# Optimization experiments

Hardware: AMD Instinct MI355X
Metric: run time of the kernel (lower is better)

## Reference

```python
import jax, jax.numpy as jnp
import numpy as np

N_NODES = 50000
N_HEDGES = 100000
E = 800000          # node->node incidences and hedge->node incidences
F_IN = 128
F_H = 64
F_OUT = 128


def setup_inputs() -> dict:
    key = jax.random.key(0)
    ks = jax.random.split(key, 10)
    node_features = jax.random.normal(ks[0], (N_NODES, F_IN), jnp.float32)
    hedge_features = jax.random.normal(ks[1], (N_HEDGES, F_H), jnp.float32)
    node_senders = jax.random.randint(ks[2], (E,), 0, N_NODES)
    node_receivers = jnp.sort(jax.random.randint(ks[3], (E,), 0, N_NODES))
    node_convolution = jax.random.uniform(ks[4], (E, 1), jnp.float32)
    hedge2node_senders = jax.random.randint(ks[5], (E,), 0, N_HEDGES)
    hedge2node_receivers = jnp.sort(jax.random.randint(ks[6], (E,), 0, N_NODES))
    hedge2node_convolution = jax.random.uniform(ks[7], (E, 1), jnp.float32)
    # eqx.nn.Linear-style uniform init: U(-1/sqrt(fan_in), 1/sqrt(fan_in))
    lim1 = 1.0 / np.sqrt(F_IN)
    lim2 = 1.0 / np.sqrt(F_H)
    W_msg = jax.random.uniform(ks[8], (F_OUT, F_IN), jnp.float32, -lim1, lim1)
    b_msg = jnp.zeros((F_OUT,), jnp.float32)
    W_scale = jax.random.uniform(ks[9], (F_OUT, F_H), jnp.float32, -lim2, lim2)
    b_scale = jnp.zeros((F_OUT,), jnp.float32)
    return dict(node_features=node_features, hedge_features=hedge_features,
                node_senders=node_senders, node_receivers=node_receivers,
                node_convolution=node_convolution,
                hedge2node_senders=hedge2node_senders,
                hedge2node_receivers=hedge2node_receivers,
                hedge2node_convolution=hedge2node_convolution,
                W_msg=W_msg, b_msg=b_msg, W_scale=W_scale, b_scale=b_scale)


def reference(node_features, hedge_features, node_senders, node_receivers,
              node_convolution, hedge2node_senders, hedge2node_receivers,
              hedge2node_convolution, W_msg, b_msg, W_scale, b_scale):
    # pipeline 1: gather node senders -> linear -> scale -> scatter-add to receivers
    sender_features = node_features[node_senders]                 # [E, F_IN]
    messages = sender_features @ W_msg.T + b_msg                  # [E, F_OUT]
    gathered_messages = jax.ops.segment_sum(
        node_convolution * messages, node_receivers, num_segments=N_NODES)
    # pipeline 2: gather hedge senders -> linear -> scale -> scatter-add to receivers
    hedge_sender_features = hedge_features[hedge2node_senders]    # [E, F_H]
    hedge_messages = hedge_sender_features @ W_scale.T + b_scale  # [E, F_OUT]
    gathered_scaling = jax.ops.segment_sum(
        hedge2node_convolution * hedge_messages, hedge2node_receivers,
        num_segments=N_NODES)
    return jnp.tanh(gathered_scaling * gathered_messages)         # [N_NODES, F_OUT]
```

## Files before the change

### kernel.cpp

```cpp
#include <hip/hip_runtime.h>

#define N_NODES   50000
#define N_HEDGES  100000
#define E_EDGES   800000
#define F_IN      128
#define F_H       64
#define F_OUT     128

typedef __attribute__((ext_vector_type(8))) short short8;
typedef __attribute__((ext_vector_type(4))) float f32x4;
typedef _Float16 half2_t __attribute__((ext_vector_type(2)));
typedef _Float16 half4_t __attribute__((ext_vector_type(4)));

__device__ __forceinline__ unsigned short f2bf(float f) {
    unsigned int u = __float_as_uint(f);
    return (unsigned short)((u + 0x7fffu + ((u >> 16) & 1u)) >> 16);
}
__device__ __forceinline__ float bf2f(unsigned short h) {
    return __uint_as_float(((unsigned int)h) << 16);
}

#define OFF_ITEMS (2 * (N_NODES + 1) + F_OUT * (F_IN + F_H))
#define OFF_B     ((OFF_ITEMS + 255) / 256)
#define CONV_NODE_F4  (N_NODES * 32)
#define CONV_HEDGE_F4 (N_HEDGES * 16)
#define CONV_B    ((CONV_NODE_F4 + CONV_HEDGE_F4 + 255) / 256)

__global__ __launch_bounds__(256)
void offsets_kernel(const int* __restrict__ recv1, const int* __restrict__ recv2,
                    int* __restrict__ offs1, int* __restrict__ offs2,
                    const float* __restrict__ Wm, const float* __restrict__ Wsc,
                    unsigned short* __restrict__ wmhi, unsigned short* __restrict__ wmlo,
                    unsigned short* __restrict__ wshi, unsigned short* __restrict__ wslo,
                    const float* __restrict__ nf, const float* __restrict__ hf,
                    _Float16* __restrict__ nfH, _Float16* __restrict__ hfH) {
    if (blockIdx.x < OFF_B) {
        int t = blockIdx.x * blockDim.x + threadIdx.x;
        const int total = N_NODES + 1;
        if (t < total) {
            int r = t, lo = 0, hi = E_EDGES;
            while (lo < hi) { int mid = (lo + hi) >> 1; if (recv1[mid] < r) lo = mid + 1; else hi = mid; }
            offs1[r] = lo;
        } else if (t < 2 * total) {
            int r = t - total, lo = 0, hi = E_EDGES;
            while (lo < hi) { int mid = (lo + hi) >> 1; if (recv2[mid] < r) lo = mid + 1; else hi = mid; }
            offs2[r] = lo;
        } else if (t < OFF_ITEMS) {
            int idx = t - 2 * total;
            if (idx < F_OUT * F_IN) {
                float f = Wm[idx];
                unsigned short h = f2bf(f);
                wmhi[idx] = h; wmlo[idx] = f2bf(f - bf2f(h));
            } else {
                int i2 = idx - F_OUT * F_IN;
                float f = Wsc[i2];
                unsigned short h = f2bf(f);
                wshi[i2] = h; wslo[i2] = f2bf(f - bf2f(h));
            }
        }
    } else {
        int idx = (blockIdx.x - OFF_B) * 256 + threadIdx.x;
        if (idx < CONV_NODE_F4) {
            float4 v = *(const float4*)(nf + (size_t)idx * 4);
            half4_t h = { (_Float16)v.x, (_Float16)v.y, (_Float16)v.z, (_Float16)v.w };
            *(half4_t*)(nfH + (size_t)idx * 4) = h;
        } else {
            int i2 = idx - CONV_NODE_F4;
            if (i2 < CONV_HEDGE_F4) {
                float4 v = *(const float4*)(hf + (size_t)i2 * 4);
                half4_t h = { (_Float16)v.x, (_Float16)v.y, (_Float16)v.z, (_Float16)v.w };
                *(half4_t*)(hfH + (size_t)i2 * 4) = h;
            }
        }
    }
}

__device__ __forceinline__ void node4(const _Float16* base, const int* __restrict__ snd,
                                      const float* __restrict__ cv, int i,
                                      float& a0, float& a1, float& cs) {
    int   s0 = snd[i],  s1 = snd[i+1], s2 = snd[i+2], s3 = snd[i+3];
    float c0 = cv[i],   c1 = cv[i+1],  c2 = cv[i+2],  c3 = cv[i+3];
    half2_t v0 = *(const half2_t*)(base + (size_t)s0 * F_IN);
    half2_t v1 = *(const half2_t*)(base + (size_t)s1 * F_IN);
    half2_t v2 = *(const half2_t*)(base + (size_t)s2 * F_IN);
    half2_t v3 = *(const half2_t*)(base + (size_t)s3 * F_IN);
    a0 += c0 * (float)v0.x; a1 += c0 * (float)v0.y;
    a0 += c1 * (float)v1.x; a1 += c1 * (float)v1.y;
    a0 += c2 * (float)v2.x; a1 += c2 * (float)v2.y;
    a0 += c3 * (float)v3.x; a1 += c3 * (float)v3.y;
    cs += c0 + c1 + c2 + c3;
}
__device__ __forceinline__ void node1(const _Float16* base, const int* __restrict__ snd,
                                      const float* __restrict__ cv, int i,
                                      float& a0, float& a1, float& cs) {
    int sn = snd[i]; float c = cv[i];
    half2_t v = *(const half2_t*)(base + (size_t)sn * F_IN);
    a0 += c * (float)v.x; a1 += c * (float)v.y; cs += c;
}
__device__ __forceinline__ void hedge4(const _Float16* base, const int* __restrict__ snd,
                                       const float* __restrict__ cv, int i,
                                       float& a, float& cs) {
    int   s0 = snd[i],  s1 = snd[i+1], s2 = snd[i+2], s3 = snd[i+3];
    float c0 = cv[i],   c1 = cv[i+1],  c2 = cv[i+2],  c3 = cv[i+3];
    float v0 = (float)base[(size_t)s0 * F_H], v1 = (float)base[(size_t)s1 * F_H];
    float v2 = (float)base[(size_t)s2 * F_H], v3 = (float)base[(size_t)s3 * F_H];
    a += c0 * v0; a += c1 * v1; a += c2 * v2; a += c3 * v3;
    cs += c0 + c1 + c2 + c3;
}
__device__ __forceinline__ void hedge1(const _Float16* base, const int* __restrict__ snd,
                                       const float* __restrict__ cv, int i,
                                       float& a, float& cs) {
    int sn = snd[i]; float c = cv[i];
    a += c * (float)base[(size_t)sn * F_H]; cs += c;
}
__device__ __forceinline__ void pack_node(char* a1pack, int node, int lane, float a0, float a1) {
    unsigned short h0 = f2bf(a0), h1 = f2bf(a1);
    unsigned short l0 = f2bf(a0 - bf2f(h0)), l1 = f2bf(a1 - bf2f(h1));
    *(unsigned int*)(a1pack + (size_t)node * 512 + lane * 4)       = (unsigned)h0 | ((unsigned)h1 << 16);
    *(unsigned int*)(a1pack + (size_t)node * 512 + 256 + lane * 4) = (unsigned)l0 | ((unsigned)l1 << 16);
}
__device__ __forceinline__ void pack_hedge(char* a2pack, int node, int lane, float a) {
    unsigned short h = f2bf(a);
    unsigned short l = f2bf(a - bf2f(h));
    ((unsigned short*)(a2pack + (size_t)node * 256))[lane]       = h;
    ((unsigned short*)(a2pack + (size_t)node * 256 + 128))[lane] = l;
}

__global__ __launch_bounds__(256)
void gather_fused(const _Float16* __restrict__ nfH, const _Float16* __restrict__ hfH,
                  const int* __restrict__ snd1, const float* __restrict__ cv1,
                  const int* __restrict__ o1,
                  const int* __restrict__ snd2, const float* __restrict__ cv2,
                  const int* __restrict__ o2,
                  char* a1pack, char* __restrict__ a2pack,
                  float* __restrict__ cs1o, float* __restrict__ cs2o) {
    const int lane = threadIdx.x & 63;
    const int wid  = threadIdx.x >> 6;
    const int NB   = N_NODES / 8;

    if (blockIdx.x < NB) {
        const int nodeA = blockIdx.x * 8 + wid * 2;
        const int nodeB = nodeA + 1;
        const _Float16* base = nfH + lane * 2;
        int iA = o1[nodeA];
        int eA = o1[nodeB];
        int iB = eA;
        int eB = o1[nodeB + 1];
        float aA0 = 0.f, aA1 = 0.f, csA = 0.f;
        float aB0 = 0.f, aB1 = 0.f, csB = 0.f;
        while (iA + 4 <= eA && iB + 4 <= eB) {
            node4(base, snd1, cv1, iA, aA0, aA1, csA);
            node4(base, snd1, cv1, iB, aB0, aB1, csB);
            iA += 4; iB += 4;
        }
        for (; iA + 4 <= eA; iA += 4) node4(base, snd1, cv1, iA, aA0, aA1, csA);
        for (; iA < eA; ++iA)         node1(base, snd1, cv1, iA, aA0, aA1, csA);
        for (; iB + 4 <= eB; iB += 4) node4(base, snd1, cv1, iB, aB0, aB1, csB);
        for (; iB < eB; ++iB)         node1(base, snd1, cv1, iB, aB0, aB1, csB);
        pack_node(a1pack, nodeA, lane, aA0, aA1);
        pack_node(a1pack, nodeB, lane, aB0, aB1);
        if (lane == 0) { cs1o[nodeA] = csA; cs1o[nodeB] = csB; }
    } else {
        const int nodeA = (blockIdx.x - NB) * 8 + wid * 2;
        const int nodeB = nodeA + 1;
        const _Float16* base = hfH + lane;
        int iA = o2[nodeA];
        int eA = o2[nodeB];
        int iB = eA;
        int eB = o2[nodeB + 1];
        float aA = 0.f, csA = 0.f, aB = 0.f, csB = 0.f;
        while (iA + 4 <= eA && iB + 4 <= eB) {
            hedge4(base, snd2, cv2, iA, aA, csA);
            hedge4(base, snd2, cv2, iB, aB, csB);
            iA += 4; iB += 4;
        }
        for (; iA + 4 <= eA; iA += 4) hedge4(base, snd2, cv2, iA, aA, csA);
        for (; iA < eA; ++iA)         hedge1(base, snd2, cv2, iA, aA, csA);
        for (; iB + 4 <= eB; iB += 4) hedge4(base, snd2, cv2, iB, aB, csB);
        for (; iB < eB; ++iB)         hedge1(base, snd2, cv2, iB, aB, csB);
        pack_hedge(a2pack, nodeA, lane, aA);
        pack_hedge(a2pack, nodeB, lane, aB);
        if (lane == 0) { cs2o[nodeA] = csA; cs2o[nodeB] = csB; }
    }
}

__global__ __launch_bounds__(256)
void gather_nodes_kernel(const float* __restrict__ nf, const int* __restrict__ senders,
                         const float* __restrict__ conv, const int* __restrict__ offs,
                         char* a1pack, float* __restrict__ csum_out) {
    const int lane = threadIdx.x & 63;
    const int node = blockIdx.x * 4 + (threadIdx.x >> 6);
    const int s = offs[node], e = offs[node + 1];
    float a0 = 0.f, a1 = 0.f, cs = 0.f;
    const float* base = nf + lane * 2;
    int i = s;
    for (; i + 4 <= e; i += 4) {
        int   s0 = senders[i],   s1 = senders[i+1], s2 = senders[i+2], s3 = senders[i+3];
        float c0 = conv[i],      c1 = conv[i+1],    c2 = conv[i+2],    c3 = conv[i+3];
        float2 v0 = *(const float2*)(base + s0 * F_IN);
        float2 v1 = *(const float2*)(base + s1 * F_IN);
        float2 v2 = *(const float2*)(base + s2 * F_IN);
        float2 v3 = *(const float2*)(base + s3 * F_IN);
        a0 += c0 * v0.x; a1 += c0 * v0.y;
        a0 += c1 * v1.x; a1 += c1 * v1.y;
        a0 += c2 * v2.x; a1 += c2 * v2.y;
        a0 += c3 * v3.x; a1 += c3 * v3.y;
        cs += c0 + c1 + c2 + c3;
    }
    for (; i < e; ++i) {
        int sn = senders[i]; float c = conv[i];
        float2 v = *(const float2*)(base + sn * F_IN);
        a0 += c * v.x; a1 += c * v.y; cs += c;
    }
    unsigned short h0 = f2bf(a0), h1 = f2bf(a1);
    unsigned short l0 = f2bf(a0 - bf2f(h0)), l1 = f2bf(a1 - bf2f(h1));
    unsigned int* hp = (unsigned int*)(a1pack + (size_t)node * 512);
    unsigned int* lp = (unsigned int*)(a1pack + (size_t)node * 512 + 256);
    hp[lane] = (unsigned int)h0 | ((unsigned int)h1 << 16);
    lp[lane] = (unsigned int)l0 | ((unsigned int)l1 << 16);
    if (lane == 0) csum_out[node] = cs;
}

__global__ __launch_bounds__(256)
void gather_hedges_kernel(const float* __restrict__ hf, const int* __restrict__ senders,
                          const float* __restrict__ conv, const int* __restrict__ offs,
                          char* __restrict__ a2pack, float* __restrict__ csum_out) {
    const int lane = threadIdx.x & 63;
    const int node = blockIdx.x * 4 + (threadIdx.x >> 6);
    const int s = offs[node], e = offs[node + 1];
    float a = 0.f, cs = 0.f;
    const float* base = hf + lane;
    int i = s;
    for (; i + 4 <= e; i += 4) {
        int   s0 = senders[i],   s1 = senders[i+1], s2 = senders[i+2], s3 = senders[i+3];
        float c0 = conv[i],      c1 = conv[i+1],    c2 = conv[i+2],    c3 = conv[i+3];
        float v0 = base[s0 * F_H], v1 = base[s1 * F_H];
        float v2 = base[s2 * F_H], v3 = base[s3 * F_H];
        a += c0 * v0; a += c1 * v1; a += c2 * v2; a += c3 * v3;
        cs += c0 + c1 + c2 + c3;
    }
    for (; i < e; ++i) {
        int sn = senders[i]; float c = conv[i];
        a += c * base[sn * F_H]; cs += c;
    }
    unsigned short h = f2bf(a);
    unsigned short l = f2bf(a - bf2f(h));
    ((unsigned short*)(a2pack + (size_t)node * 256))[lane]       = h;
    ((unsigned short*)(a2pack + (size_t)node * 256 + 128))[lane] = l;
    if (lane == 0) csum_out[node] = cs;
}

__global__ __launch_bounds__(256)
void gemm_tanh_kernel(const char* a1pack,
                      const char* __restrict__ a2pack,
                      const float* __restrict__ csum1, const float* __restrict__ csum2,
                      const unsigned short* __restrict__ wmhi, const unsigned short* __restrict__ wmlo,
                      const unsigned short* __restrict__ wshi, const unsigned short* __restrict__ wslo,
                      const float* __restrict__ bm, const float* __restrict__ bs,
                      float* outp) {
    __shared__ __align__(16) char sA1[16 * 512];
    __shared__ __align__(16) char sA2[16 * 256];
    __shared__ float sCs[16][2];

    const int t   = threadIdx.x;
    const int wid = t >> 6;
    const int l   = t & 63;
    const int g   = l >> 4;
    const int jl  = l & 15;

    short8 wm_h[2][4], wm_l[2][4], ws_h[2][2], ws_l[2][2];
    float bmj[2], bsj[2];
    #pragma unroll
    for (int jt = 0; jt < 2; ++jt) {
        const int j = wid * 32 + jt * 16 + jl;
        #pragma unroll
        for (int ks = 0; ks < 4; ++ks) {
            wm_h[jt][ks] = *(const short8*)(wmhi + j * F_IN + ks * 32 + g * 8);
            wm_l[jt][ks] = *(const short8*)(wmlo + j * F_IN + ks * 32 + g * 8);
        }
        #pragma unroll
        for (int ks = 0; ks < 2; ++ks) {
            ws_h[jt][ks] = *(const short8*)(wshi + j * F_H + ks * 32 + g * 8);
            ws_l[jt][ks] = *(const short8*)(wslo + j * F_H + ks * 32 + g * 8);
        }
        bmj[jt] = bm[j]; bsj[jt] = bs[j];
    }

    #pragma unroll 1
    for (int ns = 0; ns < 4; ++ns) {
        const int n0 = blockIdx.x * 64 + ns * 16;
        #pragma unroll
        for (int it = 0; it < 2; ++it) {
            int fi = (it << 8) + t;
            int ci = fi & 31, row = fi >> 5;
            int nsrc = min(n0 + row, N_NODES - 1);
            float4 v = *(const float4*)(a1pack + (size_t)nsrc * 512 + ci * 16);
            *(float4*)(sA1 + row * 512 + (((unsigned)ci << 4) ^ (((unsigned)row & 7) << 4))) = v;
        }
        {
            int ci = t & 15, row = t >> 4;
            int nsrc = min(n0 + row, N_NODES - 1);
            float4 v = *(const float4*)(a2pack + (size_t)nsrc * 256 + ci * 16);
            *(float4*)(sA2 + row * 256 + (((unsigned)ci << 4) ^ (((unsigned)row & 7) << 4))) = v;
        }
        if (t < 16)      sCs[t][0]      = csum1[min(n0 + t, N_NODES - 1)];
        else if (t < 32) sCs[t - 16][1] = csum2[min(n0 + t - 16, N_NODES - 1)];
        __syncthreads();

        short8 a1h[4], a1l[4], a2h[2], a2l[2];
        const unsigned sw = ((unsigned)jl & 7) << 4;
        #pragma unroll
        for (int ks = 0; ks < 4; ++ks) {
            unsigned cc = (((unsigned)(4 * ks + g)) << 4) ^ sw;
            a1h[ks] = *(const short8*)(sA1 + jl * 512 + cc);
            a1l[ks] = *(const short8*)(sA1 + jl * 512 + 256 + cc);
        }
        #pragma unroll
        for (int ks = 0; ks < 2; ++ks) {
            unsigned cc = (((unsigned)(4 * ks + g)) << 4) ^ sw;
            a2h[ks] = *(const short8*)(sA2 + jl * 256 + cc);
            a2l[ks] = *(const short8*)(sA2 + jl * 256 + 128 + cc);
        }

        #pragma unroll
        for (int jt = 0; jt < 2; ++jt) {
            f32x4 c1 = {0.f, 0.f, 0.f, 0.f}, c2 = {0.f, 0.f, 0.f, 0.f};
            #pragma unroll
            for (int ks = 0; ks < 4; ++ks) {
                c1 = __builtin_amdgcn_mfma_f32_16x16x32_bf16(a1h[ks], wm_h[jt][ks], c1, 0, 0, 0);
                c1 = __builtin_amdgcn_mfma_f32_16x16x32_bf16(a1h[ks], wm_l[jt][ks], c1, 0, 0, 0);
                c1 = __builtin_amdgcn_mfma_f32_16x16x32_bf16(a1l[ks], wm_h[jt][ks], c1, 0, 0, 0);
            }
            #pragma unroll
            for (int ks = 0; ks < 2; ++ks) {
                c2 = __builtin_amdgcn_mfma_f32_16x16x32_bf16(a2h[ks], ws_h[jt][ks], c2, 0, 0, 0);
                c2 = __builtin_amdgcn_mfma_f32_16x16x32_bf16(a2h[ks], ws_l[jt][ks], c2, 0, 0, 0);
                c2 = __builtin_amdgcn_mfma_f32_16x16x32_bf16(a2l[ks], ws_h[jt][ks], c2, 0, 0, 0);
            }
            const int j = wid * 32 + jt * 16 + jl;
            #pragma unroll
            for (int r = 0; r < 4; ++r) {
                int row  = g * 4 + r;
                int node = n0 + row;
                if (node < N_NODES) {
                    float v1 = c1[r] + sCs[row][0] * bmj[jt];
                    float v2 = c2[r] + sCs[row][1] * bsj[jt];
                    outp[(size_t)node * F_OUT + j] = tanhf(v1 * v2);
                }
            }
        }
        __syncthreads();
    }
}

extern "C" void kernel_launch(void* const* d_in, const int* in_sizes, int n_in,
                              void* d_out, int out_size, void* d_ws, size_t ws_size,
                              hipStream_t stream) {
    const float* node_features  = (const float*)d_in[0];
    const float* hedge_features = (const float*)d_in[1];
    const int*   node_senders   = (const int*)d_in[2];
    const int*   node_receivers = (const int*)d_in[3];
    const float* node_conv      = (const float*)d_in[4];
    const int*   h2n_senders    = (const int*)d_in[5];
    const int*   h2n_receivers  = (const int*)d_in[6];
    const float* h2n_conv       = (const float*)d_in[7];
    const float* W_msg          = (const float*)d_in[8];
    const float* b_msg          = (const float*)d_in[9];
    const float* W_scale        = (const float*)d_in[10];
    const float* b_scale        = (const float*)d_in[11];

    float* out = (float*)d_out;
    char*  ws  = (char*)d_ws;

    char*  A2pack = ws;
    float* Csum1  = (float*)(ws + 12800000);
    float* Csum2  = (float*)(ws + 13000000);
    int*   offs1  = (int*)  (ws + 13200000);
    int*   offs2  = (int*)  (ws + 13400016);
    unsigned short* wmhi = (unsigned short*)(ws + 13600032);
    unsigned short* wmlo = (unsigned short*)(ws + 13632800);
    unsigned short* wshi = (unsigned short*)(ws + 13665568);
    unsigned short* wslo = (unsigned short*)(ws + 13681952);
    _Float16* nfH = (_Float16*)(ws + 13698560);
    _Float16* hfH = (_Float16*)(ws + 26498560);
    const size_t WS_NEED_FAST = 39298560;
    char*  A1pack = (char*)d_out;

    const bool fast = (ws_size >= WS_NEED_FAST);

    if (fast) {
        offsets_kernel<<<OFF_B + CONV_B, 256, 0, stream>>>(
            node_receivers, h2n_receivers, offs1, offs2,
            W_msg, W_scale, wmhi, wmlo, wshi, wslo,
            node_features, hedge_features, nfH, hfH);
        gather_fused<<<2 * (N_NODES / 8), 256, 0, stream>>>(
            nfH, hfH,
            node_senders, node_conv, offs1,
            h2n_senders, h2n_conv, offs2,
            A1pack, A2pack, Csum1, Csum2);
    } else {
        offsets_kernel<<<OFF_B, 256, 0, stream>>>(
            node_receivers, h2n_receivers, offs1, offs2,
            W_msg, W_scale, wmhi, wmlo, wshi, wslo,
            node_features, hedge_features, nfH, hfH);
        gather_nodes_kernel<<<N_NODES / 4, 256, 0, stream>>>(
            node_features, node_senders, node_conv, offs1, A1pack, Csum1);
        gather_hedges_kernel<<<N_NODES / 4, 256, 0, stream>>>(
            hedge_features, h2n_senders, h2n_conv, offs2, A2pack, Csum2);
    }

    gemm_tanh_kernel<<<(N_NODES + 63) / 64, 256, 0, stream>>>(
        A1pack, A2pack, Csum1, Csum2, wmhi, wmlo, wshi, wslo,
        b_msg, b_scale, out);
}
```

Before: 111.3 us.

## Pack sender index and conv weight into 64-bit edge records, gather four nodes per wave

The prologue kernel now interleaves each edge's sender index and convolution weight into one 64-bit word. The gather kernel reads these with nontemporal loads instead of two separate scalar streams. Each wave now processes four receiver nodes concurrently instead of two, to expose more independent gathers in flight. The cost is an extra pass writing about 12.8 MB of packed edge data, plus more register pressure from the wider interleave, which can lower occupancy.

After: 135.9 us. +22.2%, slower.

```diff
diff --git a/kernel.cpp b/kernel.cpp
--- a/kernel.cpp
+++ b/kernel.cpp
@@ -24,7 +24,9 @@
 #define OFF_B     ((OFF_ITEMS + 255) / 256)
 #define CONV_NODE_F4  (N_NODES * 32)
 #define CONV_HEDGE_F4 (N_HEDGES * 16)
-#define CONV_B    ((CONV_NODE_F4 + CONV_HEDGE_F4 + 255) / 256)
+#define CONV_ITEMS (CONV_NODE_F4 + CONV_HEDGE_F4)
+#define EM_ITEMS   (2 * E_EDGES)
+#define TAIL_B  ((CONV_ITEMS + EM_ITEMS + 255) / 256)
 
 __global__ __launch_bounds__(256)
 void offsets_kernel(const int* __restrict__ recv1, const int* __restrict__ recv2,
@@ -33,7 +35,11 @@
                     unsigned short* __restrict__ wmhi, unsigned short* __restrict__ wmlo,
                     unsigned short* __restrict__ wshi, unsigned short* __restrict__ wslo,
                     const float* __restrict__ nf, const float* __restrict__ hf,
-                    _Float16* __restrict__ nfH, _Float16* __restrict__ hfH) {
+                    _Float16* __restrict__ nfH, _Float16* __restrict__ hfH,
+                    const int* __restrict__ snd1, const float* __restrict__ cv1,
+                    const int* __restrict__ snd2, const float* __restrict__ cv2,
+                    unsigned long long* __restrict__ em1,
+                    unsigned long long* __restrict__ em2) {
     if (blockIdx.x < OFF_B) {
         int t = blockIdx.x * blockDim.x + threadIdx.x;
         const int total = N_NODES + 1;
@@ -64,54 +70,78 @@
             float4 v = *(const float4*)(nf + (size_t)idx * 4);
             half4_t h = { (_Float16)v.x, (_Float16)v.y, (_Float16)v.z, (_Float16)v.w };
             *(half4_t*)(nfH + (size_t)idx * 4) = h;
+        } else if (idx < CONV_ITEMS) {
+            int i2 = idx - CONV_NODE_F4;
+            float4 v = *(const float4*)(hf + (size_t)i2 * 4);
+            half4_t h = { (_Float16)v.x, (_Float16)v.y, (_Float16)v.z, (_Float16)v.w };
+            *(half4_t*)(hfH + (size_t)i2 * 4) = h;
         } else {
-            int i2 = idx - CONV_NODE_F4;
-            if (i2 < CONV_HEDGE_F4) {
-                float4 v = *(const float4*)(hf + (size_t)i2 * 4);
-                half4_t h = { (_Float16)v.x, (_Float16)v.y, (_Float16)v.z, (_Float16)v.w };
-                *(half4_t*)(hfH + (size_t)i2 * 4) = h;
+            int k = idx - CONV_ITEMS;
+            if (k < E_EDGES) {
+                em1[k] = ((unsigned long long)__float_as_uint(cv1[k]) << 32)
+                       | (unsigned int)snd1[k];
+            } else {
+                int k2 = k - E_EDGES;
+                em2[k2] = ((unsigned long long)__float_as_uint(cv2[k2]) << 32)
+                        | (unsigned int)snd2[k2];
             }
         }
     }
 }
 
-__device__ __forceinline__ void node4(const _Float16* base, const int* __restrict__ snd,
-                                      const float* __restrict__ cv, int i,
-                                      float& a0, float& a1, float& cs) {
-    int   s0 = snd[i],  s1 = snd[i+1], s2 = snd[i+2], s3 = snd[i+3];
-    float c0 = cv[i],   c1 = cv[i+1],  c2 = cv[i+2],  c3 = cv[i+3];
-    half2_t v0 = *(const half2_t*)(base + (size_t)s0 * F_IN);
-    half2_t v1 = *(const half2_t*)(base + (size_t)s1 * F_IN);
-    half2_t v2 = *(const half2_t*)(base + (size_t)s2 * F_IN);
-    half2_t v3 = *(const half2_t*)(base + (size_t)s3 * F_IN);
+__device__ __forceinline__ void node4em(const _Float16* base,
+                                        const unsigned long long* __restrict__ em, int i,
+                                        float& a0, float& a1, float& cs) {
+    unsigned long long m0 = __builtin_nontemporal_load(em + i);
+    unsigned long long m1 = __builtin_nontemporal_load(em + i + 1);
+    unsigned long long m2 = __builtin_nontemporal_load(em + i + 2);
+    unsigned long long m3 = __builtin_nontemporal_load(em + i + 3);
+    float c0 = __uint_as_float((unsigned)(m0 >> 32));
+    float c1 = __uint_as_float((unsigned)(m1 >> 32));
+    float c2 = __uint_as_float((unsigned)(m2 >> 32));
+    float c3 = __uint_as_float((unsigned)(m3 >> 32));
+    half2_t v0 = *(const half2_t*)(base + (size_t)(unsigned)m0 * F_IN);
+    half2_t v1 = *(const half2_t*)(base + (size_t)(unsigned)m1 * F_IN);
+    half2_t v2 = *(const half2_t*)(base + (size_t)(unsigned)m2 * F_IN);
+    half2_t v3 = *(const half2_t*)(base + (size_t)(unsigned)m3 * F_IN);
     a0 += c0 * (float)v0.x; a1 += c0 * (float)v0.y;
     a0 += c1 * (float)v1.x; a1 += c1 * (float)v1.y;
     a0 += c2 * (float)v2.x; a1 += c2 * (float)v2.y;
     a0 += c3 * (float)v3.x; a1 += c3 * (float)v3.y;
     cs += c0 + c1 + c2 + c3;
 }
-__device__ __forceinline__ void node1(const _Float16* base, const int* __restrict__ snd,
-                                      const float* __restrict__ cv, int i,
-                                      float& a0, float& a1, float& cs) {
-    int sn = snd[i]; float c = cv[i];
-    half2_t v = *(const half2_t*)(base + (size_t)sn * F_IN);
+__device__ __forceinline__ void node1em(const _Float16* base,
+                                        const unsigned long long* __restrict__ em, int i,
+                                        float& a0, float& a1, float& cs) {
+    unsigned long long m = __builtin_nontemporal_load(em + i);
+    float c = __uint_as_float((unsigned)(m >> 32));
+    half2_t v = *(const half2_t*)(base + (size_t)(unsigned)m * F_IN);
     a0 += c * (float)v.x; a1 += c * (float)v.y; cs += c;
 }
-__device__ __forceinline__ void hedge4(const _Float16* base, const int* __restrict__ snd,
-                                       const float* __restrict__ cv, int i,
-                                       float& a, float& cs) {
-    int   s0 = snd[i],  s1 = snd[i+1], s2 = snd[i+2], s3 = snd[i+3];
-    float c0 = cv[i],   c1 = cv[i+1],  c2 = cv[i+2],  c3 = cv[i+3];
-    float v0 = (float)base[(size_t)s0 * F_H], v1 = (float)base[(size_t)s1 * F_H];
-    float v2 = (float)base[(size_t)s2 * F_H], v3 = (float)base[(size_t)s3 * F_H];
+__device__ __forceinline__ void hedge4em(const _Float16* base,
+                                         const unsigned long long* __restrict__ em, int i,
+                                         float& a, float& cs) {
+    unsigned long long m0 = __builtin_nontemporal_load(em + i);
+    unsigned long long m1 = __builtin_nontemporal_load(em + i + 1);
+    unsigned long long m2 = __builtin_nontemporal_load(em + i + 2);
+    unsigned long long m3 = __builtin_nontemporal_load(em + i + 3);
+    float c0 = __uint_as_float((unsigned)(m0 >> 32));
+    float c1 = __uint_as_float((unsigned)(m1 >> 32));
+    float c2 = __uint_as_float((unsigned)(m2 >> 32));
+    float c3 = __uint_as_float((unsigned)(m3 >> 32));
+    float v0 = (float)base[(size_t)(unsigned)m0 * F_H];
+    float v1 = (float)base[(size_t)(unsigned)m1 * F_H];
+    float v2 = (float)base[(size_t)(unsigned)m2 * F_H];
+    float v3 = (float)base[(size_t)(unsigned)m3 * F_H];
     a += c0 * v0; a += c1 * v1; a += c2 * v2; a += c3 * v3;
     cs += c0 + c1 + c2 + c3;
 }
-__device__ __forceinline__ void hedge1(const _Float16* base, const int* __restrict__ snd,
-                                       const float* __restrict__ cv, int i,
-                                       float& a, float& cs) {
-    int sn = snd[i]; float c = cv[i];
-    a += c * (float)base[(size_t)sn * F_H]; cs += c;
+__device__ __forceinline__ void hedge1em(const _Float16* base,
+                                         const unsigned long long* __restrict__ em, int i,
+                                         float& a, float& cs) {
+    unsigned long long m = __builtin_nontemporal_load(em + i);
+    float c = __uint_as_float((unsigned)(m >> 32));
+    a += c * (float)base[(size_t)(unsigned)m * F_H]; cs += c;
 }
 __device__ __forceinline__ void pack_node(char* a1pack, int node, int lane, float a0, float a1) {
     unsigned short h0 = f2bf(a0), h1 = f2bf(a1);
@@ -128,59 +158,84 @@
 
 __global__ __launch_bounds__(256)
 void gather_fused(const _Float16* __restrict__ nfH, const _Float16* __restrict__ hfH,
-                  const int* __restrict__ snd1, const float* __restrict__ cv1,
+                  const unsigned long long* __restrict__ em1,
                   const int* __restrict__ o1,
-                  const int* __restrict__ snd2, const float* __restrict__ cv2,
+                  const unsigned long long* __restrict__ em2,
                   const int* __restrict__ o2,
                   char* a1pack, char* __restrict__ a2pack,
                   float* __restrict__ cs1o, float* __restrict__ cs2o) {
     const int lane = threadIdx.x & 63;
     const int wid  = threadIdx.x >> 6;
-    const int NB   = N_NODES / 8;
+    const int NB   = N_NODES / 16;
 
     if (blockIdx.x < NB) {
-        const int nodeA = blockIdx.x * 8 + wid * 2;
-        const int nodeB = nodeA + 1;
+        const int n0 = blockIdx.x * 16 + wid * 4;
         const _Float16* base = nfH + lane * 2;
-        int iA = o1[nodeA];
-        int eA = o1[nodeB];
-        int iB = eA;
-        int eB = o1[nodeB + 1];
-        float aA0 = 0.f, aA1 = 0.f, csA = 0.f;
-        float aB0 = 0.f, aB1 = 0.f, csB = 0.f;
-        while (iA + 4 <= eA && iB + 4 <= eB) {
-            node4(base, snd1, cv1, iA, aA0, aA1, csA);
-            node4(base, snd1, cv1, iB, aB0, aB1, csB);
-            iA += 4; iB += 4;
-        }
-        for (; iA + 4 <= eA; iA += 4) node4(base, snd1, cv1, iA, aA0, aA1, csA);
-        for (; iA < eA; ++iA)         node1(base, snd1, cv1, iA, aA0, aA1, csA);
-        for (; iB + 4 <= eB; iB += 4) node4(base, snd1, cv1, iB, aB0, aB1, csB);
-        for (; iB < eB; ++iB)         node1(base, snd1, cv1, iB, aB0, aB1, csB);
-        pack_node(a1pack, nodeA, lane, aA0, aA1);
-        pack_node(a1pack, nodeB, lane, aB0, aB1);
-        if (lane == 0) { cs1o[nodeA] = csA; cs1o[nodeB] = csB; }
+        int o[5];
+        #pragma unroll
+        for (int k = 0; k < 5; ++k) o[k] = o1[n0 + k];
+        int i0 = o[0], e0 = o[1], i1 = o[1], e1 = o[2];
+        int i2 = o[2], e2 = o[3], i3 = o[3], e3 = o[4];
+        float a00 = 0.f, a01 = 0.f, cs0 = 0.f;
+        float a10 = 0.f, a11 = 0.f, cs1 = 0.f;
+        float a20 = 0.f, a21 = 0.f, cs2 = 0.f;
+        float a30 = 0.f, a31 = 0.f, cs3 = 0.f;
+        while (i0 + 4 <= e0 && i1 + 4 <= e1 && i2 + 4 <= e2 && i3 + 4 <= e3) {
+            node4em(base, em1, i0, a00, a01, cs0);
+            node4em(base, em1, i1, a10, a11, cs1);
+            node4em(base, em1, i2, a20, a21, cs2);
+            node4em(base, em1, i3, a30, a31, cs3);
+            i0 += 4; i1 += 4; i2 += 4; i3 += 4;
+        }
+        for (; i0 + 4 <= e0; i0 += 4) node4em(base, em1, i0, a00, a01, cs0);
+        for (; i0 < e0; ++i0)         node1em(base, em1, i0, a00, a01, cs0);
+        for (; i1 + 4 <= e1; i1 += 4) node4em(base, em1, i1, a10, a11, cs1);
+        for (; i1 < e1; ++i1)         node1em(base, em1, i1, a10, a11, cs1);
+        for (; i2 + 4 <= e2; i2 += 4) node4em(base, em1, i2, a20, a21, cs2);
+        for (; i2 < e2; ++i2)         node1em(base, em1, i2, a20, a21, cs2);
+        for (; i3 + 4 <= e3; i3 += 4) node4em(base, em1, i3, a30, a31, cs3);
+        for (; i3 < e3; ++i3)         node1em(base, em1, i3, a30, a31, cs3);
+        pack_node(a1pack, n0 + 0, lane, a00, a01);
+        pack_node(a1pack, n0 + 1, lane, a10, a11);
+        pack_node(a1pack, n0 + 2, lane, a20, a21);
+        pack_node(a1pack, n0 + 3, lane, a30, a31);
+        if (lane == 0) {
+            cs1o[n0 + 0] = cs0; cs1o[n0 + 1] = cs1;
+            cs1o[n0 + 2] = cs2; cs1o[n0 + 3] = cs3;
+        }
     } else {
-        const int nodeA = (blockIdx.x - NB) * 8 + wid * 2;
-        const int nodeB = nodeA + 1;
+        const int n0 = (blockIdx.x - NB) * 16 + wid * 4;
         const _Float16* base = hfH + lane;
-        int iA = o2[nodeA];
-        int eA = o2[nodeB];
-        int iB = eA;
-        int eB = o2[nodeB + 1];
-        float aA = 0.f, csA = 0.f, aB = 0.f, csB = 0.f;
-        while (iA + 4 <= eA && iB + 4 <= eB) {
-            hedge4(base, snd2, cv2, iA, aA, csA);
-            hedge4(base, snd2, cv2, iB, aB, csB);
-            iA += 4; iB += 4;
-        }
-        for (; iA + 4 <= eA; iA += 4) hedge4(base, snd2, cv2, iA, aA, csA);
-        for (; iA < eA; ++iA)         hedge1(base, snd2, cv2, iA, aA, csA);
-        for (; iB + 4 <= eB; iB += 4) hedge4(base, snd2, cv2, iB, aB, csB);
-        for (; iB < eB; ++iB)         hedge1(base, snd2, cv2, iB, aB, csB);
-        pack_hedge(a2pack, nodeA, lane, aA);
-        pack_hedge(a2pack, nodeB, lane, aB);
-        if (lane == 0) { cs2o[nodeA] = csA; cs2o[nodeB] = csB; }
+        int o[5];
+        #pragma unroll
+        for (int k = 0; k < 5; ++k) o[k] = o2[n0 + k];
+        int i0 = o[0], e0 = o[1], i1 = o[1], e1 = o[2];
+        int i2 = o[2], e2 = o[3], i3 = o[3], e3 = o[4];
+        float a0 = 0.f, cs0 = 0.f, a1 = 0.f, cs1 = 0.f;
+        float a2 = 0.f, cs2 = 0.f, a3 = 0.f, cs3 = 0.f;
+        while (i0 + 4 <= e0 && i1 + 4 <= e1 && i2 + 4 <= e2 && i3 + 4 <= e3) {
+            hedge4em(base, em2, i0, a0, cs0);
+            hedge4em(base, em2, i1, a1, cs1);
+            hedge4em(base, em2, i2, a2, cs2);
+            hedge4em(base, em2, i3, a3, cs3);
+            i0 += 4; i1 += 4; i2 += 4; i3 += 4;
+        }
+        for (; i0 + 4 <= e0; i0 += 4) hedge4em(base, em2, i0, a0, cs0);
+        for (; i0 < e0; ++i0)         hedge1em(base, em2, i0, a0, cs0);
+        for (; i1 + 4 <= e1; i1 += 4) hedge4em(base, em2, i1, a1, cs1);
+        for (; i1 < e1; ++i1)         hedge1em(base, em2, i1, a1, cs1);
+        for (; i2 + 4 <= e2; i2 += 4) hedge4em(base, em2, i2, a2, cs2);
+        for (; i2 < e2; ++i2)         hedge1em(base, em2, i2, a2, cs2);
+        for (; i3 + 4 <= e3; i3 += 4) hedge4em(base, em2, i3, a3, cs3);
+        for (; i3 < e3; ++i3)         hedge1em(base, em2, i3, a3, cs3);
+        pack_hedge(a2pack, n0 + 0, lane, a0);
+        pack_hedge(a2pack, n0 + 1, lane, a1);
+        pack_hedge(a2pack, n0 + 2, lane, a2);
+        pack_hedge(a2pack, n0 + 3, lane, a3);
+        if (lane == 0) {
+            cs2o[n0 + 0] = cs0; cs2o[n0 + 1] = cs1;
+            cs2o[n0 + 2] = cs2; cs2o[n0 + 3] = cs3;
+        }
     }
 }
 
@@ -383,26 +438,28 @@
     unsigned short* wslo = (unsigned short*)(ws + 13681952);
     _Float16* nfH = (_Float16*)(ws + 13698560);
     _Float16* hfH = (_Float16*)(ws + 26498560);
-    const size_t WS_NEED_FAST = 39298560;
+    unsigned long long* em1 = (unsigned long long*)(ws + 39298560);
+    unsigned long long* em2 = (unsigned long long*)(ws + 45698560);
+    const size_t WS_NEED_FAST = 52098560;
     char*  A1pack = (char*)d_out;
 
     const bool fast = (ws_size >= WS_NEED_FAST);
 
     if (fast) {
-        offsets_kernel<<<OFF_B + CONV_B, 256, 0, stream>>>(
+        offsets_kernel<<<OFF_B + TAIL_B, 256, 0, stream>>>(
             node_receivers, h2n_receivers, offs1, offs2,
             W_msg, W_scale, wmhi, wmlo, wshi, wslo,
-            node_features, hedge_features, nfH, hfH);
-        gather_fused<<<2 * (N_NODES / 8), 256, 0, stream>>>(
-            nfH, hfH,
-            node_senders, node_conv, offs1,
-            h2n_senders, h2n_conv, offs2,
+            node_features, hedge_features, nfH, hfH,
+            node_senders, node_conv, h2n_senders, h2n_conv, em1, em2);
+        gather_fused<<<2 * (N_NODES / 16), 256, 0, stream>>>(
+            nfH, hfH, em1, offs1, em2, offs2,
             A1pack, A2pack, Csum1, Csum2);
     } else {
         offsets_kernel<<<OFF_B, 256, 0, stream>>>(
             node_receivers, h2n_receivers, offs1, offs2,
             W_msg, W_scale, wmhi, wmlo, wshi, wslo,
-            node_features, hedge_features, nfH, hfH);
+            node_features, hedge_features, nfH, hfH,
+            node_senders, node_conv, h2n_senders, h2n_conv, em1, em2);
         gather_nodes_kernel<<<N_NODES / 4, 256, 0, stream>>>(
             node_features, node_senders, node_conv, offs1, A1pack, Csum1);
         gather_hedges_kernel<<<N_NODES / 4, 256, 0, stream>>>(
```
